# Kernel tuning notes

Hardware: AMD Instinct MI355X
Metric: run time of the kernel (lower is better)

## Reference

```python
import jax, jax.numpy as jnp
import numpy as np

ALPHA = 32.0
RANK = 16


def setup_inputs() -> dict:
    key = jax.random.key(0)
    ks = jax.random.split(key, 5)
    in_f, out_f = 1024, 1024
    x = jax.random.normal(ks[0], (8, 8192, in_f), dtype=jnp.float32)
    W = jax.random.normal(ks[1], (out_f, in_f), dtype=jnp.float32) * 0.02  # base weight [out, in]
    bias = jax.random.normal(ks[2], (out_f,), dtype=jnp.float32) * 0.02
    B = jax.random.normal(ks[3], (in_f, RANK), dtype=jnp.float32) * 0.05   # delta_weight_B
    A = jax.random.normal(ks[4], (RANK, out_f), dtype=jnp.float32) * 0.05  # delta_weight_A
    return {"x": x, "W": W, "bias": bias, "B": B, "A": A}


def reference(x, W, bias, B, A):
    # Faithful to: x @ (W.T + alpha/rank * (B @ A)) + bias  (adapter enabled)
    scale = jnp.float32(ALPHA / RANK)
    eff_weight = W.T + scale * jnp.matmul(B, A)  # [in, out]
    return jnp.matmul(x, eff_weight) + bias
```

## Files before the change

### kernel.cpp

```cpp
#include <hip/hip_runtime.h>
#include <hip/hip_bf16.h>


typedef short short8 __attribute__((ext_vector_type(8)));
typedef float f32x4 __attribute__((ext_vector_type(4)));

#define K_DIM 1024
#define N_DIM 1024
#define BM 256
#define BN 256
#define BK 64
#define NT (K_DIM / BK)

static __device__ __forceinline__ unsigned short f2bf_rne(float v) {
    unsigned u = __builtin_bit_cast(unsigned, v);
    u += 0x7fffu + ((u >> 16) & 1u);
    return (unsigned short)(u >> 16);
}

static __device__ __forceinline__ int pack_bf16x2(float a, float b) {
    __hip_bfloat162 h = __float22bfloat162_rn(make_float2(a, b));
    int r;
    __builtin_memcpy(&r, &h, sizeof(r));
    return r;
}

__global__ __launch_bounds__(256) void weff_kernel(
    const float* __restrict__ W, const float* __restrict__ B,
    const float* __restrict__ A, unsigned short* __restrict__ WeffT) {
    int idx = blockIdx.x * 256 + threadIdx.x;
    int n = idx >> 10;
    int k = idx & 1023;
    const float4* Bk = (const float4*)(B + k * 16);
    float s = 0.f;
#pragma unroll
    for (int r4 = 0; r4 < 4; ++r4) {
        float4 b4 = Bk[r4];
        s += b4.x * A[(r4 * 4 + 0) * N_DIM + n];
        s += b4.y * A[(r4 * 4 + 1) * N_DIM + n];
        s += b4.z * A[(r4 * 4 + 2) * N_DIM + n];
        s += b4.w * A[(r4 * 4 + 3) * N_DIM + n];
    }
    float v = W[idx] + 2.0f * s;
    WeffT[idx] = f2bf_rne(v);
}

__global__ __launch_bounds__(512, 2) void lora_gemm(
    const float* __restrict__ X, const unsigned short* __restrict__ WeffT,
    const float* __restrict__ bias, float* __restrict__ Out) {
    __shared__ short As[2][BM * BK];
    __shared__ short Bs[2][BN * BK];

    const int t = threadIdx.x;
    const int lane = t & 63;
    const int w = t >> 6;
    const int quad = lane >> 4;
    const int l15 = lane & 15;
    const int wm = w >> 2;
    const int wc = w & 3;

    const int bid = blockIdx.x;
    const int wgid = (bid & 7) * 128 + (bid >> 3);
    const int m_tile = wgid >> 2;
    const int n_tile = wgid & 3;
    const size_t m_base = (size_t)m_tile * BM;
    const int n_base = n_tile * BN;

    const int trow = t >> 3;
    const int tc = t & 7;
    const int tswz = tc ^ (trow & 7);
    const float* asrc0 = X + (m_base + trow) * K_DIM + tc * 8;
    const unsigned short* bsrc0 = WeffT + (size_t)(n_base + trow) * K_DIM + tswz * 8;
    const int aw_base = trow * BK + tswz * 8;

    const int a_base = (wm * 128 + l15) * BK;
    const int b_base = (wc * 64 + l15) * BK;
    const int sw0 = (quad ^ (l15 & 7)) * 8;
    const int sw1 = ((4 + quad) ^ (l15 & 7)) * 8;

    f32x4 acc[8][4];
#pragma unroll
    for (int mi = 0; mi < 8; ++mi)
#pragma unroll
        for (int ni = 0; ni < 4; ++ni)
            acc[mi][ni] = (f32x4){0.f, 0.f, 0.f, 0.f};

    f32x4 rA[8];

#define ISSUE_B(pp, koff)                                                           \
    do {                                                                            \
        _Pragma("unroll") for (int i = 0; i < 4; ++i) {                             \
            __builtin_amdgcn_global_load_lds(                                       \
                (const __attribute__((address_space(1))) unsigned int*)(            \
                    bsrc0 + i * 64 * K_DIM + (koff)),                               \
                (__attribute__((address_space(3))) unsigned int*)                   \
                    &Bs[pp][w * 512 + i * 4096],                                    \
                16, 0, 0);                                                          \
        }                                                                           \
    } while (0)

#define ISSUE_A(koff)                                                               \
    do {                                                                            \
        _Pragma("unroll") for (int i = 0; i < 4; ++i) {                             \
            const f32x4* gp = (const f32x4*)(asrc0 + i * 64 * K_DIM + (koff));      \
            rA[2 * i] = gp[0];                                                      \
            rA[2 * i + 1] = gp[1];                                                  \
        }                                                                           \
    } while (0)

#define CVT_WRITE(pp)                                                               \
    do {                                                                            \
        _Pragma("unroll") for (int i = 0; i < 4; ++i) {                             \
            int4 wv;                                                                \
            wv.x = pack_bf16x2(rA[2 * i][0], rA[2 * i][1]);                         \
            wv.y = pack_bf16x2(rA[2 * i][2], rA[2 * i][3]);                         \
            wv.z = pack_bf16x2(rA[2 * i + 1][0], rA[2 * i + 1][1]);                 \
            wv.w = pack_bf16x2(rA[2 * i + 1][2], rA[2 * i + 1][3]);                 \
            *(int4*)&As[pp][aw_base + i * 4096] = wv;                               \
        }                                                                           \
    } while (0)

#define COMPUTE(pp, swv)                                                            \
    do {                                                                            \
        short8 af[8], bf[4];                                                        \
        _Pragma("unroll") for (int mi = 0; mi < 8; ++mi)                            \
            af[mi] = *(const short8*)&As[pp][a_base + mi * 1024 + (swv)];           \
        _Pragma("unroll") for (int ni = 0; ni < 4; ++ni)                            \
            bf[ni] = *(const short8*)&Bs[pp][b_base + ni * 1024 + (swv)];           \
        __builtin_amdgcn_s_setprio(1);                                              \
        _Pragma("unroll") for (int mi = 0; mi < 8; ++mi)                            \
            _Pragma("unroll") for (int ni = 0; ni < 4; ++ni)                        \
                acc[mi][ni] = __builtin_amdgcn_mfma_f32_16x16x32_bf16(              \
                    af[mi], bf[ni], acc[mi][ni], 0, 0, 0);                          \
        __builtin_amdgcn_s_setprio(0);                                              \
    } while (0)

    ISSUE_B(0, 0);
    ISSUE_A(0);
    asm volatile("s_waitcnt vmcnt(0)" ::: "memory");
    CVT_WRITE(0);
    ISSUE_A(BK);
    asm volatile("s_waitcnt lgkmcnt(0)" ::: "memory");
    __builtin_amdgcn_s_barrier();

#pragma unroll 2
    for (int s = 0; s < NT; ++s) {
        const int p = s & 1;
        if (s + 1 < NT) ISSUE_B(p ^ 1, (s + 1) * BK);
        COMPUTE(p, sw0);
        if (s + 1 < NT) {
            asm volatile("s_waitcnt vmcnt(4)" ::: "memory");
            CVT_WRITE(p ^ 1);
            if (s + 2 < NT) ISSUE_A((s + 2) * BK);
        }
        COMPUTE(p, sw1);
        if (s + 1 < NT) {
            if (s + 2 < NT)
                asm volatile("s_waitcnt vmcnt(8) lgkmcnt(0)" ::: "memory");
            else
                asm volatile("s_waitcnt vmcnt(0) lgkmcnt(0)" ::: "memory");
            __builtin_amdgcn_s_barrier();
        }
    }

#undef ISSUE_B
#undef ISSUE_A
#undef CVT_WRITE
#undef COMPUTE

#pragma unroll
    for (int ni = 0; ni < 4; ++ni) {
        const int col = n_base + wc * 64 + ni * 16 + l15;
        const float bv = bias[col];
#pragma unroll
        for (int mi = 0; mi < 8; ++mi) {
            const size_t row0 = m_base + wm * 128 + mi * 16 + quad * 4;
#pragma unroll
            for (int r = 0; r < 4; ++r)
                Out[(row0 + r) * N_DIM + col] = acc[mi][ni][r] + bv;
        }
    }
}

extern "C" void kernel_launch(void* const* d_in, const int* in_sizes, int n_in,
                              void* d_out, int out_size, void* d_ws, size_t ws_size,
                              hipStream_t stream) {
    const float* x    = (const float*)d_in[0];
    const float* W    = (const float*)d_in[1];
    const float* bias = (const float*)d_in[2];
    const float* B    = (const float*)d_in[3];
    const float* A    = (const float*)d_in[4];
    float* out = (float*)d_out;
    unsigned short* WeffT = (unsigned short*)d_ws;

    weff_kernel<<<4096, 256, 0, stream>>>(W, B, A, WeffT);

    int M = out_size / N_DIM;
    int grid = (M / BM) * (N_DIM / BN);
    lora_gemm<<<grid, 512, 0, stream>>>(x, WeffT, bias, out);
}
```

Before: 615.0 us.

## Restructure GEMM main loop into 8-phase ping-pong schedule with split LDS halves

Splits the LDS A/B tiles into 128-row halves and restructures the K loop into eight fine-grained phases per two K-tiles, each loading a quarter of fragments, barriering, then issuing MFMAs. Global loads, bf16 conversion writes and async LDS loads for the next tile are interleaved between phases with explicit waitcnt gates and sched_barriers. The aim is HipKittens-style overlap of memory and compute across the two co-resident waves. It adds many more workgroup barriers, which may cost throughput if the phases are not balanced.

```diff
diff --git a/kernel.cpp b/kernel.cpp
--- a/kernel.cpp
+++ b/kernel.cpp
@@ -10,7 +10,6 @@
 #define BM 256
 #define BN 256
 #define BK 64
-#define NT (K_DIM / BK)
 
 static __device__ __forceinline__ unsigned short f2bf_rne(float v) {
     unsigned u = __builtin_bit_cast(unsigned, v);
@@ -48,8 +47,8 @@
 __global__ __launch_bounds__(512, 2) void lora_gemm(
     const float* __restrict__ X, const unsigned short* __restrict__ WeffT,
     const float* __restrict__ bias, float* __restrict__ Out) {
-    __shared__ short As[2][BM * BK];
-    __shared__ short Bs[2][BN * BK];
+    __shared__ short As[2][2][128 * 64];
+    __shared__ short Bs[2][2][128 * 64];
 
     const int t = threadIdx.x;
     const int lane = t & 63;
@@ -58,6 +57,7 @@
     const int l15 = lane & 15;
     const int wm = w >> 2;
     const int wc = w & 3;
+    const int bh = wc >> 1;
 
     const int bid = blockIdx.x;
     const int wgid = (bid & 7) * 128 + (bid >> 3);
@@ -68,15 +68,17 @@
 
     const int trow = t >> 3;
     const int tc = t & 7;
-    const int tswz = tc ^ (trow & 7);
-    const float* asrc0 = X + (m_base + trow) * K_DIM + tc * 8;
-    const unsigned short* bsrc0 = WeffT + (size_t)(n_base + trow) * K_DIM + tswz * 8;
-    const int aw_base = trow * BK + tswz * 8;
-
-    const int a_base = (wm * 128 + l15) * BK;
-    const int b_base = (wc * 64 + l15) * BK;
+    const int awc = (tc ^ (trow & 7)) * 8;
+    const float* asrc_base = X + (m_base + trow) * K_DIM + tc * 8;
+    const unsigned short* bsrc_base =
+        WeffT + (size_t)(n_base + trow) * K_DIM + (size_t)(tc ^ (trow & 7)) * 8;
+
     const int sw0 = (quad ^ (l15 & 7)) * 8;
     const int sw1 = ((4 + quad) ^ (l15 & 7)) * 8;
+    const int a_off0 = l15 * 64 + sw0;
+    const int a_off1 = l15 * 64 + sw1;
+    const int b_off0 = (wc & 1) * 4096 + l15 * 64 + sw0;
+    const int b_off1 = (wc & 1) * 4096 + l15 * 64 + sw1;
 
     f32x4 acc[8][4];
 #pragma unroll
@@ -87,86 +89,131 @@
 
     f32x4 rA[8];
 
-#define ISSUE_B(pp, koff)                                                           \
-    do {                                                                            \
-        _Pragma("unroll") for (int i = 0; i < 4; ++i) {                             \
+#define FENCE asm volatile("" ::: "memory")
+
+#define ISSUE_B(PB, H, koff)                                                        \
+    do {                                                                            \
+        _Pragma("unroll") for (int j = 0; j < 2; ++j) {                             \
             __builtin_amdgcn_global_load_lds(                                       \
                 (const __attribute__((address_space(1))) unsigned int*)(            \
-                    bsrc0 + i * 64 * K_DIM + (koff)),                               \
+                    bsrc_base + (size_t)((H) * 128 + j * 64) * K_DIM + (koff)),     \
                 (__attribute__((address_space(3))) unsigned int*)                   \
-                    &Bs[pp][w * 512 + i * 4096],                                    \
+                    &Bs[PB][H][(j * 512 + w * 64) * 8],                             \
                 16, 0, 0);                                                          \
         }                                                                           \
     } while (0)
 
-#define ISSUE_A(koff)                                                               \
-    do {                                                                            \
-        _Pragma("unroll") for (int i = 0; i < 4; ++i) {                             \
-            const f32x4* gp = (const f32x4*)(asrc0 + i * 64 * K_DIM + (koff));      \
-            rA[2 * i] = gp[0];                                                      \
-            rA[2 * i + 1] = gp[1];                                                  \
-        }                                                                           \
-    } while (0)
-
-#define CVT_WRITE(pp)                                                               \
-    do {                                                                            \
-        _Pragma("unroll") for (int i = 0; i < 4; ++i) {                             \
+#define ISSUE_A(H, koff)                                                            \
+    do {                                                                            \
+        _Pragma("unroll") for (int i = 0; i < 2; ++i) {                             \
+            const f32x4* gp = (const f32x4*)(asrc_base +                            \
+                (size_t)((H) * 128 + i * 64) * K_DIM + (koff));                     \
+            rA[(H) * 4 + 2 * i] = gp[0];                                            \
+            rA[(H) * 4 + 2 * i + 1] = gp[1];                                        \
+        }                                                                           \
+    } while (0)
+
+#define CVT_WRITE(PB, H)                                                            \
+    do {                                                                            \
+        _Pragma("unroll") for (int i = 0; i < 2; ++i) {                             \
             int4 wv;                                                                \
-            wv.x = pack_bf16x2(rA[2 * i][0], rA[2 * i][1]);                         \
-            wv.y = pack_bf16x2(rA[2 * i][2], rA[2 * i][3]);                         \
-            wv.z = pack_bf16x2(rA[2 * i + 1][0], rA[2 * i + 1][1]);                 \
-            wv.w = pack_bf16x2(rA[2 * i + 1][2], rA[2 * i + 1][3]);                 \
-            *(int4*)&As[pp][aw_base + i * 4096] = wv;                               \
-        }                                                                           \
-    } while (0)
-
-#define COMPUTE(pp, swv)                                                            \
-    do {                                                                            \
-        short8 af[8], bf[4];                                                        \
-        _Pragma("unroll") for (int mi = 0; mi < 8; ++mi)                            \
-            af[mi] = *(const short8*)&As[pp][a_base + mi * 1024 + (swv)];           \
-        _Pragma("unroll") for (int ni = 0; ni < 4; ++ni)                            \
-            bf[ni] = *(const short8*)&Bs[pp][b_base + ni * 1024 + (swv)];           \
+            wv.x = pack_bf16x2(rA[(H)*4 + 2*i][0], rA[(H)*4 + 2*i][1]);             \
+            wv.y = pack_bf16x2(rA[(H)*4 + 2*i][2], rA[(H)*4 + 2*i][3]);             \
+            wv.z = pack_bf16x2(rA[(H)*4 + 2*i + 1][0], rA[(H)*4 + 2*i + 1][1]);     \
+            wv.w = pack_bf16x2(rA[(H)*4 + 2*i + 1][2], rA[(H)*4 + 2*i + 1][3]);     \
+            *(int4*)&As[PB][H][(i * 64 + trow) * 64 + awc] = wv;                    \
+        }                                                                           \
+    } while (0)
+
+#define PHASE_CORE(PB, MH, NH)                                                      \
+    do {                                                                            \
+        short8 af0[4], af1[4], bf0[2], bf1[2];                                      \
+        _Pragma("unroll") for (int mi = 0; mi < 4; ++mi) {                          \
+            af0[mi] = *(const short8*)&As[PB][wm][(MH)*4096 + mi*1024 + a_off0];    \
+            af1[mi] = *(const short8*)&As[PB][wm][(MH)*4096 + mi*1024 + a_off1];    \
+        }                                                                           \
+        _Pragma("unroll") for (int ni = 0; ni < 2; ++ni) {                          \
+            bf0[ni] = *(const short8*)&Bs[PB][bh][(NH)*2048 + ni*1024 + b_off0];    \
+            bf1[ni] = *(const short8*)&Bs[PB][bh][(NH)*2048 + ni*1024 + b_off1];    \
+        }                                                                           \
+        asm volatile("s_waitcnt lgkmcnt(0)" ::: "memory");                          \
+        __builtin_amdgcn_sched_barrier(0);                                          \
+        __builtin_amdgcn_s_barrier();                                               \
         __builtin_amdgcn_s_setprio(1);                                              \
-        _Pragma("unroll") for (int mi = 0; mi < 8; ++mi)                            \
-            _Pragma("unroll") for (int ni = 0; ni < 4; ++ni)                        \
-                acc[mi][ni] = __builtin_amdgcn_mfma_f32_16x16x32_bf16(              \
-                    af[mi], bf[ni], acc[mi][ni], 0, 0, 0);                          \
+        _Pragma("unroll") for (int mi = 0; mi < 4; ++mi)                            \
+            _Pragma("unroll") for (int ni = 0; ni < 2; ++ni) {                      \
+                acc[(MH)*4+mi][(NH)*2+ni] = __builtin_amdgcn_mfma_f32_16x16x32_bf16(\
+                    af0[mi], bf0[ni], acc[(MH)*4+mi][(NH)*2+ni], 0, 0, 0);          \
+                acc[(MH)*4+mi][(NH)*2+ni] = __builtin_amdgcn_mfma_f32_16x16x32_bf16(\
+                    af1[mi], bf1[ni], acc[(MH)*4+mi][(NH)*2+ni], 0, 0, 0);          \
+            }                                                                       \
         __builtin_amdgcn_s_setprio(0);                                              \
     } while (0)
 
-    ISSUE_B(0, 0);
-    ISSUE_A(0);
-    asm volatile("s_waitcnt vmcnt(0)" ::: "memory");
-    CVT_WRITE(0);
-    ISSUE_A(BK);
+#define PHASE_END __builtin_amdgcn_s_barrier()
+#define GATE4 do { asm volatile("s_waitcnt vmcnt(4)" ::: "memory"); \
+                   __builtin_amdgcn_sched_barrier(0); } while (0)
+#define GATE0 do { asm volatile("s_waitcnt vmcnt(0)" ::: "memory"); \
+                   __builtin_amdgcn_sched_barrier(0); } while (0)
+
+    ISSUE_A(0, 0);
+    ISSUE_A(1, 0);
+    FENCE;
+    ISSUE_B(0, 0, 0);
+    FENCE;
+    CVT_WRITE(0, 0);
+    FENCE;
+    ISSUE_A(0, 64);
+    FENCE;
+    CVT_WRITE(0, 1);
+    FENCE;
+    ISSUE_B(0, 1, 0);
+    FENCE;
+    ISSUE_A(1, 64);
+    FENCE;
+    GATE4;
     asm volatile("s_waitcnt lgkmcnt(0)" ::: "memory");
+    __builtin_amdgcn_sched_barrier(0);
     __builtin_amdgcn_s_barrier();
 
-#pragma unroll 2
-    for (int s = 0; s < NT; ++s) {
-        const int p = s & 1;
-        if (s + 1 < NT) ISSUE_B(p ^ 1, (s + 1) * BK);
-        COMPUTE(p, sw0);
-        if (s + 1 < NT) {
-            asm volatile("s_waitcnt vmcnt(4)" ::: "memory");
-            CVT_WRITE(p ^ 1);
-            if (s + 2 < NT) ISSUE_A((s + 2) * BK);
-        }
-        COMPUTE(p, sw1);
-        if (s + 1 < NT) {
-            if (s + 2 < NT)
-                asm volatile("s_waitcnt vmcnt(8) lgkmcnt(0)" ::: "memory");
-            else
-                asm volatile("s_waitcnt vmcnt(0) lgkmcnt(0)" ::: "memory");
-            __builtin_amdgcn_s_barrier();
-        }
-    }
-
+#pragma unroll 1
+    for (int u = 0; u < 7; ++u) {
+        const int kt = u * 128;
+        CVT_WRITE(1, 0); FENCE; ISSUE_B(1, 0, kt + 64); FENCE; ISSUE_A(0, kt + 128); FENCE;
+        PHASE_CORE(0, 0, 0); PHASE_END;
+        CVT_WRITE(1, 1); FENCE; ISSUE_B(1, 1, kt + 64); FENCE; ISSUE_A(1, kt + 128); FENCE;
+        PHASE_CORE(0, 0, 1); PHASE_END;
+        PHASE_CORE(0, 1, 0); PHASE_END;
+        PHASE_CORE(0, 1, 1); GATE4; PHASE_END;
+        CVT_WRITE(0, 0); FENCE; ISSUE_B(0, 0, kt + 128); FENCE; ISSUE_A(0, kt + 192); FENCE;
+        PHASE_CORE(1, 0, 0); PHASE_END;
+        CVT_WRITE(0, 1); FENCE; ISSUE_B(0, 1, kt + 128); FENCE; ISSUE_A(1, kt + 192); FENCE;
+        PHASE_CORE(1, 0, 1); PHASE_END;
+        PHASE_CORE(1, 1, 0); PHASE_END;
+        PHASE_CORE(1, 1, 1); GATE4; PHASE_END;
+    }
+
+    {
+        CVT_WRITE(1, 0); FENCE; ISSUE_B(1, 0, 960); FENCE;
+        PHASE_CORE(0, 0, 0); PHASE_END;
+        CVT_WRITE(1, 1); FENCE; ISSUE_B(1, 1, 960); FENCE;
+        PHASE_CORE(0, 0, 1); PHASE_END;
+        PHASE_CORE(0, 1, 0); PHASE_END;
+        PHASE_CORE(0, 1, 1); GATE0; PHASE_END;
+        PHASE_CORE(1, 0, 0); PHASE_END;
+        PHASE_CORE(1, 0, 1); PHASE_END;
+        PHASE_CORE(1, 1, 0); PHASE_END;
+        PHASE_CORE(1, 1, 1);
+    }
+
+#undef FENCE
 #undef ISSUE_B
 #undef ISSUE_A
 #undef CVT_WRITE
-#undef COMPUTE
+#undef PHASE_CORE
+#undef PHASE_END
+#undef GATE4
+#undef GATE0
 
 #pragma unroll
     for (int ni = 0; ni < 4; ++ni) {
```

New measurement: 614.9 us. About the same (-0.0%).
